# Performance work log

Measured on AMD Instinct MI355X. Metric: run time of the kernel, lower is better.

Reference implementation:

```python
import jax, jax.numpy as jnp
import numpy as np

B, T, D = 4, 2048, 1024
H, Kd = 4, 256                 # num_heads, head_k_dim
Vd = 512                       # head_v_dim = head_dim * expand_v
KEY_DIM, VAL_DIM = H * Kd, H * Vd
CONV = 4
EPS = 1e-6
LN_EPS = 1e-5


def _layernorm(x, g, b):
    m = jnp.mean(x, -1, keepdims=True)
    v = jnp.mean((x - m) ** 2, -1, keepdims=True)
    return (x - m) * jax.lax.rsqrt(v + LN_EPS) * g + b


def _rmsnorm(x, w):
    return x * jax.lax.rsqrt(jnp.mean(x * x, -1, keepdims=True) + EPS) * w


def _l2norm(x):
    return x * jax.lax.rsqrt(jnp.sum(x * x, -1, keepdims=True) + EPS)


def _causal_conv_silu(x, w):
    # depthwise causal conv: x [B,T,C], w [C,CONV]; y[t] = sum_i w[:,i]*x[t-(CONV-1)+i]
    t = x.shape[1]
    xp = jnp.pad(x, ((0, 0), (CONV - 1, 0), (0, 0)))
    y = xp[:, 0:t, :] * w[:, 0]
    for i in range(1, CONV):
        y = y + xp[:, i:i + t, :] * w[:, i]
    return jax.nn.silu(y)


def _gated_delta_rule(q, k, v, g, beta):
    # q,k [B,T,H,Kd] (l2-normed, q pre-scaled), v [B,T,H,Vd], g,beta [B,T,H]
    qT = jnp.moveaxis(q, 1, 0)
    kT = jnp.moveaxis(k, 1, 0)
    vT = jnp.moveaxis(v, 1, 0)
    gT = jnp.moveaxis(g, 1, 0)
    bT = jnp.moveaxis(beta, 1, 0)
    S0 = jnp.zeros((q.shape[0], H, Kd, Vd), q.dtype)

    def step(S, inp):
        q_t, k_t, v_t, g_t, b_t = inp
        S = S * jnp.exp(g_t)[..., None, None]          # decay state
        kv = jnp.einsum('bhk,bhkv->bhv', k_t, S)       # read old memory at k
        delta = (v_t - kv) * b_t[..., None]            # delta-rule update
        S = S + k_t[..., :, None] * delta[..., None, :]
        o = jnp.einsum('bhk,bhkv->bhv', q_t, S)
        return S, o

    _, o = jax.lax.scan(step, S0, (qT, kT, vT, gT, bT))
    return jnp.moveaxis(o, 0, 1)                       # [B,T,H,Vd]


def _forward(x, ln1_g, ln1_b, ln2_g, ln2_b, rms_in_w, Wq, Wk, Wv,
             conv_q_w, conv_k_w, conv_v_w, Wa, dt_bias, A_log, Wb,
             Wg, o_norm_w, Wo, W2, b2):
    b, t, _ = x.shape
    h = _layernorm(x, ln1_g, ln1_b)          # EncoderBlock norm_layer_1
    h = _rmsnorm(h, rms_in_w)                # GatedDeltaNet norm_first

    q = _causal_conv_silu(h @ Wq, conv_q_w).reshape(b, t, H, Kd)
    k = _causal_conv_silu(h @ Wk, conv_k_w).reshape(b, t, H, Kd)
    v = _causal_conv_silu(h @ Wv, conv_v_w).reshape(b, t, H, Vd)

    q = _l2norm(q) * (Kd ** -0.5)
    k = _l2norm(k)

    g = -jnp.exp(A_log) * jax.nn.softplus(h @ Wa + dt_bias)   # [B,T,H], log-decay
    beta = jax.nn.sigmoid(h @ Wb)                              # [B,T,H]

    o = _gated_delta_rule(q, k, v, g, beta)                    # [B,T,H,Vd]

    gate = (h @ Wg).reshape(b, t, H, Vd)
    o = _rmsnorm(o, o_norm_w) * jax.nn.silu(gate)              # gated RMSNorm output
    enc = o.reshape(b, t, VAL_DIM) @ Wo                        # o_proj

    x = x + enc                                                # residual
    h2 = _layernorm(x, ln2_g, ln2_b)
    x_out = jax.nn.gelu(h2 @ W2 + b2, approximate=False) + x   # stage 2 + residual
    return x_out


def setup_inputs() -> dict:
    key = jax.random.key(0)
    ks = jax.random.split(key, 16)
    r = lambda k, shp, s=0.02: jax.random.normal(k, shp, dtype=jnp.float32) * s
    return {
        'x': jax.random.normal(ks[0], (B, T, D), dtype=jnp.float32),
        'ln1_g': jnp.ones((D,), jnp.float32), 'ln1_b': jnp.zeros((D,), jnp.float32),
        'ln2_g': jnp.ones((D,), jnp.float32), 'ln2_b': jnp.zeros((D,), jnp.float32),
        'rms_in_w': jnp.ones((D,), jnp.float32),
        'Wq': r(ks[1], (D, KEY_DIM)), 'Wk': r(ks[2], (D, KEY_DIM)), 'Wv': r(ks[3], (D, VAL_DIM)),
        'conv_q_w': r(ks[4], (KEY_DIM, CONV), 0.3),
        'conv_k_w': r(ks[5], (KEY_DIM, CONV), 0.3),
        'conv_v_w': r(ks[6], (VAL_DIM, CONV), 0.3),
        'Wa': r(ks[7], (D, H)), 'dt_bias': r(ks[8], (H,), 0.5),
        'A_log': jnp.log(jax.random.uniform(ks[9], (H,), minval=1.0, maxval=16.0)),
        'Wb': r(ks[10], (D, H)),
        'Wg': r(ks[11], (D, VAL_DIM)),
        'o_norm_w': jnp.ones((Vd,), jnp.float32),
        'Wo': r(ks[12], (VAL_DIM, D)),
        'W2': r(ks[13], (D, D)), 'b2': jnp.zeros((D,), jnp.float32),
    }


def reference(x, ln1_g, ln1_b, ln2_g, ln2_b, rms_in_w, Wq, Wk, Wv,
              conv_q_w, conv_k_w, conv_v_w, Wa, dt_bias, A_log, Wb,
              Wg, o_norm_w, Wo, W2, b2):
    return _forward(x, ln1_g, ln1_b, ln2_g, ln2_b, rms_in_w, Wq, Wk, Wv,
                    conv_q_w, conv_k_w, conv_v_w, Wa, dt_bias, A_log, Wb,
                    Wg, o_norm_w, Wo, W2, b2)
```

## Files before the change

### kernel.cpp

```cpp
#include <hip/hip_runtime.h>
#include <stdint.h>

typedef uint16_t u16;
typedef __attribute__((ext_vector_type(8))) __bf16 bfrag8;
typedef __attribute__((ext_vector_type(4))) float f32x4;

#define DEV __device__ __forceinline__

DEV float bf2f(uint32_t lo16) { return __uint_as_float(lo16 << 16); }
DEV u16 f2bf(float f) {
  uint32_t u = __float_as_uint(f);
  u += 0x7fffu + ((u >> 16) & 1u);
  return (u16)(u >> 16);
}
DEV uint32_t pack2(float a, float b) { return (uint32_t)f2bf(a) | ((uint32_t)f2bf(b) << 16); }
DEV float sigmoidf_(float x) { return 1.f / (1.f + __expf(-x)); }

DEV float blk_sum(float v, float* sred, int tid) {
#pragma unroll
  for (int m = 32; m >= 1; m >>= 1) v += __shfl_xor(v, m);
  __syncthreads();
  if ((tid & 63) == 0) sred[tid >> 6] = v;
  __syncthreads();
  return sred[0] + sred[1] + sred[2] + sred[3];
}

__global__ __launch_bounds__(256) void transpose_w(const float* __restrict__ W,
                                                   u16* __restrict__ WT, int Kd_, int Nd_) {
  __shared__ float tile[32][33];
  int tx = threadIdx.x, ty = threadIdx.y;
  int n0 = blockIdx.x * 32, k0 = blockIdx.y * 32;
#pragma unroll
  for (int i = ty; i < 32; i += 8) tile[i][tx] = W[(size_t)(k0 + i) * Nd_ + n0 + tx];
  __syncthreads();
#pragma unroll
  for (int i = ty; i < 32; i += 8) WT[(size_t)(n0 + i) * Kd_ + k0 + tx] = f2bf(tile[tx][i]);
}

__global__ __launch_bounds__(256) void k1_kernel(
    const float* __restrict__ x, const float* __restrict__ ln1g, const float* __restrict__ ln1b,
    const float* __restrict__ rmsw, const float* __restrict__ Wa, const float* __restrict__ Wb,
    const float* __restrict__ dtb, const float* __restrict__ Alog,
    u16* __restrict__ hbf, float2* __restrict__ gb2) {
  __shared__ float sred[4];
  int row = blockIdx.x, tid = threadIdx.x;
  const float4 xv = ((const float4*)(x + (size_t)row * 1024))[tid];
  float ts  = blk_sum(xv.x + xv.y + xv.z + xv.w, sred, tid);
  float ts2 = blk_sum(xv.x * xv.x + xv.y * xv.y + xv.z * xv.z + xv.w * xv.w, sred, tid);
  float mean = ts * (1.f / 1024.f);
  float var  = ts2 * (1.f / 1024.f) - mean * mean;
  float inv  = rsqrtf(var + 1e-5f);
  int c = tid * 4;
  float l0 = (xv.x - mean) * inv * ln1g[c + 0] + ln1b[c + 0];
  float l1 = (xv.y - mean) * inv * ln1g[c + 1] + ln1b[c + 1];
  float l2 = (xv.z - mean) * inv * ln1g[c + 2] + ln1b[c + 2];
  float l3 = (xv.w - mean) * inv * ln1g[c + 3] + ln1b[c + 3];
  float ssq = blk_sum(l0 * l0 + l1 * l1 + l2 * l2 + l3 * l3, sred, tid);
  float rinv = rsqrtf(ssq * (1.f / 1024.f) + 1e-6f);
  float h0 = l0 * rinv * rmsw[c + 0];
  float h1 = l1 * rinv * rmsw[c + 1];
  float h2 = l2 * rinv * rmsw[c + 2];
  float h3 = l3 * rinv * rmsw[c + 3];
  uint2 pk;
  pk.x = pack2(h0, h1);
  pk.y = pack2(h2, h3);
  *(uint2*)(hbf + (size_t)row * 1024 + c) = pk;
  float hv[4] = {h0, h1, h2, h3};
  float pa[4] = {0, 0, 0, 0}, pb[4] = {0, 0, 0, 0};
#pragma unroll
  for (int e = 0; e < 4; e++) {
    const float* wa = Wa + (size_t)(c + e) * 4;
    const float* wb = Wb + (size_t)(c + e) * 4;
#pragma unroll
    for (int p = 0; p < 4; p++) {
      pa[p] = fmaf(hv[e], wa[p], pa[p]);
      pb[p] = fmaf(hv[e], wb[p], pb[p]);
    }
  }
  float ra[4], rb[4];
  for (int p = 0; p < 4; p++) ra[p] = blk_sum(pa[p], sred, tid);
  for (int p = 0; p < 4; p++) rb[p] = blk_sum(pb[p], sred, tid);
  if (tid < 4) {
    float z = ra[tid] + dtb[tid];
    float sp = fmaxf(z, 0.f) + log1pf(expf(-fabsf(z)));
    float2 o2;
    o2.x = -expf(Alog[tid]) * sp;
    o2.y = 1.f / (1.f + expf(-rb[tid]));
    gb2[(size_t)row * 4 + tid] = o2;
  }
}

template <int MODE>
__global__ __launch_bounds__(256) void gemm_bt(
    const u16* __restrict__ A, const u16* __restrict__ Bt, int M, int N, int K,
    float* __restrict__ outf, u16* __restrict__ outh,
    const float* __restrict__ res, const float* __restrict__ bias) {
  __shared__ u16 As[128 * 64];
  __shared__ u16 Bs[128 * 64];
  const int tid = threadIdx.x;
  const int lane = tid & 63;
  const int wv = tid >> 6;
  const int quad = lane >> 4;
  const int l16 = lane & 15;
  const int waveM = (wv & 1) * 64;
  const int waveN = (wv >> 1) * 64;
  const size_t arow0 = (size_t)blockIdx.y * 128;
  const size_t brow0 = (size_t)blockIdx.x * 128;
  const int srow = tid >> 3;
  const int soff = (tid & 7) * 8;
  f32x4 acc[4][4];
#pragma unroll
  for (int i = 0; i < 4; i++)
#pragma unroll
    for (int j = 0; j < 4; j++) acc[i][j] = (f32x4){0.f, 0.f, 0.f, 0.f};

  for (int k0 = 0; k0 < K; k0 += 64) {
    __syncthreads();
#pragma unroll
    for (int i = 0; i < 4; i++) {
      int r = i * 32 + srow;
      *(int4*)(As + r * 64 + soff) = *(const int4*)(A + (arow0 + r) * K + k0 + soff);
      *(int4*)(Bs + r * 64 + soff) = *(const int4*)(Bt + (brow0 + r) * K + k0 + soff);
    }
    __syncthreads();
#pragma unroll
    for (int kk = 0; kk < 2; kk++) {
      bfrag8 af[4], bfr[4];
#pragma unroll
      for (int i = 0; i < 4; i++) {
        af[i]  = *(const bfrag8*)(As + (waveM + i * 16 + l16) * 64 + kk * 32 + quad * 8);
        bfr[i] = *(const bfrag8*)(Bs + (waveN + i * 16 + l16) * 64 + kk * 32 + quad * 8);
      }
#pragma unroll
      for (int i = 0; i < 4; i++)
#pragma unroll
        for (int j = 0; j < 4; j++)
          acc[i][j] = __builtin_amdgcn_mfma_f32_16x16x32_bf16(af[i], bfr[j], acc[i][j], 0, 0, 0);
    }
  }
#pragma unroll
  for (int i = 0; i < 4; i++) {
    int r0 = (int)arow0 + waveM + i * 16 + quad * 4;
#pragma unroll
    for (int j = 0; j < 4; j++) {
      int cN = (int)brow0 + waveN + j * 16 + l16;
#pragma unroll
      for (int r = 0; r < 4; r++) {
        size_t idx = (size_t)(r0 + r) * N + cN;
        float vacc = acc[i][j][r];
        if (MODE == 0) {
          outh[idx] = f2bf(vacc);
        } else if (MODE == 1) {
          outf[idx] = vacc + res[idx];
        } else {
          float z = vacc + bias[cN];
          float ge = 0.5f * z * (1.f + erff(z * 0.70710678118654752f));
          outf[idx] = ge + res[idx];
        }
      }
    }
  }
}

__global__ __launch_bounds__(256) void conv_qk_kernel(
    const u16* __restrict__ qkv, const float* __restrict__ cwq, const float* __restrict__ cwk,
    u16* __restrict__ qf, u16* __restrict__ kf) {
  __shared__ float sred[4];
  int row = blockIdx.x, tid = threadIdx.x;
  int t = row & 2047;
  int isK = (blockIdx.y >= 4);
  int hh = blockIdx.y & 3;
  int c = hh * 256 + tid;
  const float* cw = isK ? cwk : cwq;
  int col = (isK ? 1024 : 0) + c;
  float acc = 0.f;
#pragma unroll
  for (int i = 0; i < 4; i++) {
    int tt = t - 3 + i;
    if (tt >= 0) acc = fmaf(cw[c * 4 + i], bf2f(qkv[(size_t)(row - 3 + i) * 4096 + col]), acc);
  }
  float y = acc * sigmoidf_(acc);
  float ssq = blk_sum(y * y, sred, tid);
  float r = rsqrtf(ssq + 1e-6f);
  float outv = y * r * (isK ? 1.f : 0.0625f);
  (isK ? kf : qf)[(size_t)row * 1024 + c] = f2bf(outv);
}

__global__ __launch_bounds__(256) void conv_v_kernel(
    const u16* __restrict__ qkv, const float* __restrict__ cwv, u16* __restrict__ vf) {
  int row = blockIdx.x, tid = threadIdx.x;
  int t = row & 2047;
  int c0 = blockIdx.y * 1024 + tid * 4;
  float a0 = 0, a1 = 0, a2 = 0, a3 = 0;
#pragma unroll
  for (int i = 0; i < 4; i++) {
    int tt = t - 3 + i;
    if (tt >= 0) {
      uint2 raw = *(const uint2*)(qkv + (size_t)(row - 3 + i) * 4096 + 2048 + c0);
      a0 = fmaf(cwv[(c0 + 0) * 4 + i], bf2f(raw.x & 0xffffu), a0);
      a1 = fmaf(cwv[(c0 + 1) * 4 + i], bf2f(raw.x >> 16), a1);
      a2 = fmaf(cwv[(c0 + 2) * 4 + i], bf2f(raw.y & 0xffffu), a2);
      a3 = fmaf(cwv[(c0 + 3) * 4 + i], bf2f(raw.y >> 16), a3);
    }
  }
  a0 = a0 * sigmoidf_(a0);
  a1 = a1 * sigmoidf_(a1);
  a2 = a2 * sigmoidf_(a2);
  a3 = a3 * sigmoidf_(a3);
  uint2 pk;
  pk.x = pack2(a0, a1);
  pk.y = pack2(a2, a3);
  *(uint2*)(vf + (size_t)row * 2048 + c0) = pk;
}


__global__ __launch_bounds__(256) void phaseA_kernel(
    const u16* __restrict__ kf, const u16* __restrict__ qf, const float2* __restrict__ gb2,
    u16* __restrict__ KTg, u16* __restrict__ Bg, u16* __restrict__ Mg,
    float2* __restrict__ gpk) {
  __shared__ uint8_t sm[51456];
  float* Nl  = (float*)sm;
  float* gl  = (float*)(sm + 16896);
  float* bl  = (float*)(sm + 17152);
  float* GL  = (float*)(sm + 17408);
  u16*  Klds = (u16*)(sm + 17664);
  float* Ml  = (float*)(sm + 17664);

  const int tid = threadIdx.x;
  const int lane = tid & 63;
  const int wv = tid >> 6;
  const int quad = lane >> 4;
  const int l16 = lane & 15;
  const int bh = blockIdx.x >> 5;
  const int ch = blockIdx.x & 31;
  const int b = bh >> 2, h = bh & 3;
  const int gr0 = b * 2048 + ch * 64;
  const size_t cid = (size_t)blockIdx.x;
  const size_t cid2 = (size_t)bh * 32 + ch;

  if (tid < 64) {
    float2 gv = gb2[(size_t)(gr0 + tid) * 4 + h];
    gl[tid] = gv.x; bl[tid] = gv.y;
  }
  __syncthreads();
  if (tid < 64) {
    float s = 0.f;
    for (int j = 0; j < 64; j++) { if (j <= tid) s += gl[j]; }
    GL[tid] = s;
  }
  {
    int r = tid >> 2, p = tid & 3;
    const u16* src = kf + (size_t)(gr0 + r) * 1024 + h * 256 + p * 64;
#pragma unroll
    for (int it = 0; it < 8; it++)
      *(uint4*)&Klds[r * 264 + p * 64 + it * 8] = *(const uint4*)(src + it * 8);
  }
  f32x4 ap[4], aq4[4];
#pragma unroll
  for (int nt = 0; nt < 4; nt++) { ap[nt] = (f32x4){0, 0, 0, 0}; aq4[nt] = (f32x4){0, 0, 0, 0}; }
  for (int ks = 0; ks < 8; ks++) {
    bfrag8 afk = *(const bfrag8*)(kf + (size_t)(gr0 + 16 * wv + l16) * 1024 + h * 256 + ks * 32 + quad * 8);
    bfrag8 afq = *(const bfrag8*)(qf + (size_t)(gr0 + 16 * wv + l16) * 1024 + h * 256 + ks * 32 + quad * 8);
#pragma unroll
    for (int nt = 0; nt < 4; nt++) {
      bfrag8 bfk = *(const bfrag8*)(kf + (size_t)(gr0 + 16 * nt + l16) * 1024 + h * 256 + ks * 32 + quad * 8);
      ap[nt]  = __builtin_amdgcn_mfma_f32_16x16x32_bf16(afk, bfk, ap[nt], 0, 0, 0);
      aq4[nt] = __builtin_amdgcn_mfma_f32_16x16x32_bf16(afq, bfk, aq4[nt], 0, 0, 0);
    }
  }
  __syncthreads();
#pragma unroll
  for (int nt = 0; nt < 4; nt++) {
#pragma unroll
    for (int r = 0; r < 4; r++) {
      int i = 16 * wv + quad * 4 + r;
      int j = 16 * nt + l16;
      float e = __expf(GL[i] - GL[j]);
      Nl[i * 66 + j] = (j < i) ? bl[i] * e * ap[nt][r] : 0.f;
      float bvv = (j <= i) ? e * aq4[nt][r] : 0.f;
      Bg[cid2 * 4096 + i * 64 + j] = f2bf(bvv);
    }
  }
  for (int e = 0; e < 64; e++) {
    int idx = e * 256 + tid;
    int i2 = idx & 63, k2 = idx >> 6;
    KTg[cid2 * 16384 + (size_t)k2 * 64 + i2] = Klds[i2 * 264 + k2];
  }
  if (tid < 64) {
    float2 gp;
    gp.x = __expf(GL[tid]);
    gp.y = __expf(GL[63] - GL[tid]);
    gpk[cid2 * 64 + tid] = gp;
  }
  __syncthreads();
  if (tid < 64) {
    int c = tid;
    for (int i = 0; i < 64; i++) {
      float acc = (i == c) ? bl[i] : 0.f;
      for (int j = 0; j < i; j++) acc -= Nl[i * 66 + j] * Ml[j * 66 + c];
      Ml[i * 66 + c] = acc;
    }
  }
  __syncthreads();
  for (int e = 0; e < 16; e++) {
    int idx = e * 256 + tid;
    int i2 = idx >> 6, j2 = idx & 63;
    Mg[cid2 * 4096 + i2 * 64 + j2] = f2bf(Ml[i2 * 66 + j2]);
  }
  (void)cid;
}

__global__ __launch_bounds__(256) void phaseB_kernel(
    const u16* __restrict__ kf, const u16* __restrict__ qf, const u16* __restrict__ vf,
    const u16* __restrict__ KTg, const u16* __restrict__ Bg, const u16* __restrict__ Mg,
    const float2* __restrict__ gpk, u16* __restrict__ obuf) {
  __shared__ u16 S0T[32 * 264];
  __shared__ u16 rhsT[32 * 72];
  __shared__ u16 dT[32 * 72];
  __shared__ u16 dhT[32 * 72];
  __shared__ float gin_s[64], gout_s[64];

  const int tid = threadIdx.x;
  const int lane = tid & 63;
  const int wv = tid >> 6;
  const int quad = lane >> 4;
  const int l16 = lane & 15;
  const int bh = blockIdx.x >> 4;
  const int sl = blockIdx.x & 15;
  const int b = bh >> 2, h = bh & 3;

  f32x4 S[8];
#pragma unroll
  for (int t = 0; t < 8; t++) S[t] = (f32x4){0, 0, 0, 0};

  for (int ch = 0; ch < 32; ch++) {
    const size_t cid = (size_t)bh * 32 + ch;
    const int gr0 = b * 2048 + ch * 64;
    const u16* kfc = kf + (size_t)gr0 * 1024 + h * 256;
    const u16* qfc = qf + (size_t)gr0 * 1024 + h * 256;
    const u16* vfc = vf + (size_t)gr0 * 2048 + h * 512 + sl * 32;
    u16* oc = obuf + (size_t)gr0 * 2048 + h * 512 + sl * 32;
    const u16* KTc = KTg + cid * 16384;
    const u16* Mc  = Mg + cid * 4096;
    const u16* Bc  = Bg + cid * 4096;

    if (tid < 64) {
      float2 gp = gpk[cid * 64 + tid];
      gin_s[tid] = gp.x; gout_s[tid] = gp.y;
    }
#pragma unroll
    for (int kt = 0; kt < 4; kt++)
#pragma unroll
      for (int nt = 0; nt < 2; nt++) {
        int k = wv * 64 + kt * 16 + quad * 4;
        int n = nt * 16 + l16;
        f32x4 sv = S[kt * 2 + nt];
        uint2 pk;
        pk.x = pack2(sv[0], sv[1]);
        pk.y = pack2(sv[2], sv[3]);
        *(uint2*)&S0T[n * 264 + k] = pk;
      }
    __syncthreads();

    f32x4 ar[2] = {(f32x4){0, 0, 0, 0}, (f32x4){0, 0, 0, 0}};
    for (int ks = 0; ks < 8; ks++) {
      bfrag8 af = *(const bfrag8*)(kfc + (size_t)(16 * wv + l16) * 1024 + ks * 32 + quad * 8);
#pragma unroll
      for (int nt = 0; nt < 2; nt++) {
        bfrag8 bf = *(const bfrag8*)&S0T[(nt * 16 + l16) * 264 + ks * 32 + quad * 8];
        ar[nt] = __builtin_amdgcn_mfma_f32_16x16x32_bf16(af, bf, ar[nt], 0, 0, 0);
      }
    }
#pragma unroll
    for (int nt = 0; nt < 2; nt++) {
      float rv[4];
#pragma unroll
      for (int r = 0; r < 4; r++) {
        int i = 16 * wv + quad * 4 + r;
        float vvv = bf2f(vfc[(size_t)i * 2048 + nt * 16 + l16]);
        rv[r] = vvv - gin_s[i] * ar[nt][r];
      }
      uint2 pk;
      pk.x = pack2(rv[0], rv[1]);
      pk.y = pack2(rv[2], rv[3]);
      *(uint2*)&rhsT[(nt * 16 + l16) * 72 + 16 * wv + quad * 4] = pk;
    }
    __syncthreads();

    f32x4 ad[2] = {(f32x4){0, 0, 0, 0}, (f32x4){0, 0, 0, 0}};
    for (int ks = 0; ks < 2; ks++) {
      bfrag8 af = *(const bfrag8*)(Mc + (size_t)(16 * wv + l16) * 64 + ks * 32 + quad * 8);
#pragma unroll
      for (int nt = 0; nt < 2; nt++) {
        bfrag8 bf = *(const bfrag8*)&rhsT[(nt * 16 + l16) * 72 + ks * 32 + quad * 8];
        ad[nt] = __builtin_amdgcn_mfma_f32_16x16x32_bf16(af, bf, ad[nt], 0, 0, 0);
      }
    }
#pragma unroll
    for (int nt = 0; nt < 2; nt++) {
      int i0 = 16 * wv + quad * 4;
      uint2 pk;
      pk.x = pack2(ad[nt][0], ad[nt][1]);
      pk.y = pack2(ad[nt][2], ad[nt][3]);
      *(uint2*)&dT[(nt * 16 + l16) * 72 + i0] = pk;
      uint2 pk2;
      pk2.x = pack2(gout_s[i0] * ad[nt][0], gout_s[i0 + 1] * ad[nt][1]);
      pk2.y = pack2(gout_s[i0 + 2] * ad[nt][2], gout_s[i0 + 3] * ad[nt][3]);
      *(uint2*)&dhT[(nt * 16 + l16) * 72 + i0] = pk2;
    }
    __syncthreads();

    f32x4 ao[2] = {(f32x4){0, 0, 0, 0}, (f32x4){0, 0, 0, 0}};
    for (int ks = 0; ks < 2; ks++) {
      bfrag8 af = *(const bfrag8*)(Bc + (size_t)(16 * wv + l16) * 64 + ks * 32 + quad * 8);
#pragma unroll
      for (int nt = 0; nt < 2; nt++) {
        bfrag8 bf = *(const bfrag8*)&dT[(nt * 16 + l16) * 72 + ks * 32 + quad * 8];
        ao[nt] = __builtin_amdgcn_mfma_f32_16x16x32_bf16(af, bf, ao[nt], 0, 0, 0);
      }
    }
    f32x4 aq[2] = {(f32x4){0, 0, 0, 0}, (f32x4){0, 0, 0, 0}};
    for (int ks = 0; ks < 8; ks++) {
      bfrag8 af = *(const bfrag8*)(qfc + (size_t)(16 * wv + l16) * 1024 + ks * 32 + quad * 8);
#pragma unroll
      for (int nt = 0; nt < 2; nt++) {
        bfrag8 bf = *(const bfrag8*)&S0T[(nt * 16 + l16) * 264 + ks * 32 + quad * 8];
        aq[nt] = __builtin_amdgcn_mfma_f32_16x16x32_bf16(af, bf, aq[nt], 0, 0, 0);
      }
    }
#pragma unroll
    for (int nt = 0; nt < 2; nt++)
#pragma unroll
      for (int r = 0; r < 4; r++) {
        int i = 16 * wv + quad * 4 + r;
        float ov = gin_s[i] * aq[nt][r] + ao[nt][r];
        oc[(size_t)i * 2048 + nt * 16 + l16] = f2bf(ov);
      }

    float gC = gin_s[63];
#pragma unroll
    for (int kt = 0; kt < 4; kt++) {
      f32x4 c0 = S[kt * 2] * gC;
      f32x4 c1 = S[kt * 2 + 1] * gC;
      for (int ks = 0; ks < 2; ks++) {
        bfrag8 af = *(const bfrag8*)(KTc + (size_t)(wv * 64 + kt * 16 + l16) * 64 + ks * 32 + quad * 8);
        bfrag8 bf0 = *(const bfrag8*)&dhT[(0 * 16 + l16) * 72 + ks * 32 + quad * 8];
        bfrag8 bf1 = *(const bfrag8*)&dhT[(1 * 16 + l16) * 72 + ks * 32 + quad * 8];
        c0 = __builtin_amdgcn_mfma_f32_16x16x32_bf16(af, bf0, c0, 0, 0, 0);
        c1 = __builtin_amdgcn_mfma_f32_16x16x32_bf16(af, bf1, c1, 0, 0, 0);
      }
      S[kt * 2] = c0;
      S[kt * 2 + 1] = c1;
    }
    __syncthreads();
  }
}

__global__ __launch_bounds__(256) void onorm_kernel(
    const u16* __restrict__ o, const u16* __restrict__ gate,
    const float* __restrict__ onw, u16* __restrict__ ofin) {
  __shared__ float sred[4];
  int row = blockIdx.x, hh = blockIdx.y, tid = threadIdx.x;
  size_t base = (size_t)row * 2048 + hh * 512;
  uint32_t oraw = *(const uint32_t*)(o + base + tid * 2);
  float o0 = bf2f(oraw & 0xffffu), o1 = bf2f(oraw >> 16);
  float ssq = blk_sum(o0 * o0 + o1 * o1, sred, tid);
  float rinv = rsqrtf(ssq * (1.f / 512.f) + 1e-6f);
  uint32_t graw = *(const uint32_t*)(gate + base + tid * 2);
  float g0 = bf2f(graw & 0xffffu), g1 = bf2f(graw >> 16);
  float r0 = o0 * rinv * onw[tid * 2 + 0] * (g0 * sigmoidf_(g0));
  float r1 = o1 * rinv * onw[tid * 2 + 1] * (g1 * sigmoidf_(g1));
  *(uint32_t*)(ofin + base + tid * 2) = pack2(r0, r1);
}

__global__ __launch_bounds__(256) void ln2_kernel(
    const float* __restrict__ x1, const float* __restrict__ g2, const float* __restrict__ b2,
    u16* __restrict__ h2) {
  __shared__ float sred[4];
  int row = blockIdx.x, tid = threadIdx.x;
  const float4 xv = ((const float4*)(x1 + (size_t)row * 1024))[tid];
  float ts  = blk_sum(xv.x + xv.y + xv.z + xv.w, sred, tid);
  float ts2 = blk_sum(xv.x * xv.x + xv.y * xv.y + xv.z * xv.z + xv.w * xv.w, sred, tid);
  float mean = ts * (1.f / 1024.f);
  float inv = rsqrtf(ts2 * (1.f / 1024.f) - mean * mean + 1e-5f);
  int c = tid * 4;
  float h0 = (xv.x - mean) * inv * g2[c + 0] + b2[c + 0];
  float h1 = (xv.y - mean) * inv * g2[c + 1] + b2[c + 1];
  float h2v = (xv.z - mean) * inv * g2[c + 2] + b2[c + 2];
  float h3 = (xv.w - mean) * inv * g2[c + 3] + b2[c + 3];
  uint2 pk;
  pk.x = pack2(h0, h1);
  pk.y = pack2(h2v, h3);
  *(uint2*)(h2 + (size_t)row * 1024 + c) = pk;
}

extern "C" void kernel_launch(void* const* d_in, const int* in_sizes, int n_in,
                              void* d_out, int out_size, void* d_ws, size_t ws_size,
                              hipStream_t stream) {
  (void)in_sizes; (void)n_in; (void)out_size; (void)ws_size;
  const float* x    = (const float*)d_in[0];
  const float* ln1g = (const float*)d_in[1];
  const float* ln1b = (const float*)d_in[2];
  const float* ln2g = (const float*)d_in[3];
  const float* ln2b = (const float*)d_in[4];
  const float* rmsw = (const float*)d_in[5];
  const float* Wq   = (const float*)d_in[6];
  const float* Wk   = (const float*)d_in[7];
  const float* Wv   = (const float*)d_in[8];
  const float* cwq  = (const float*)d_in[9];
  const float* cwk  = (const float*)d_in[10];
  const float* cwv  = (const float*)d_in[11];
  const float* Wa   = (const float*)d_in[12];
  const float* dtb  = (const float*)d_in[13];
  const float* Alog = (const float*)d_in[14];
  const float* Wb   = (const float*)d_in[15];
  const float* Wg   = (const float*)d_in[16];
  const float* onw  = (const float*)d_in[17];
  const float* Wo   = (const float*)d_in[18];
  const float* W2   = (const float*)d_in[19];
  const float* b2   = (const float*)d_in[20];

  uint8_t* ws = (uint8_t*)d_ws;
  const size_t MB = 1024ull * 1024;
  u16*   qkvp  = (u16*)(ws);
  u16*   obuf  = (u16*)(ws);
  u16*   KTg   = (u16*)(ws + 32 * MB);
  u16*   Bg    = (u16*)(ws + 48 * MB);
  u16*   Mg    = (u16*)(ws + 52 * MB);
  float2* gpk  = (float2*)(ws + 56 * MB);
  u16*   gate  = (u16*)(ws + 32 * MB);
  u16*   hbf   = (u16*)(ws + 64 * MB);
  u16*   WTqkv = (u16*)(ws + 80 * MB);
  u16*   WgT   = (u16*)(ws + 88 * MB);
  u16*   WoT   = (u16*)(ws + 92 * MB);
  u16*   W2T   = (u16*)(ws + 96 * MB);
  u16*   qf    = (u16*)(ws + 98 * MB);
  u16*   kf    = (u16*)(ws + 114 * MB);
  u16*   vf    = (u16*)(ws + 130 * MB);
  u16*   ofin  = (u16*)(ws + 98 * MB);
  u16*   h2bf  = (u16*)(ws + 130 * MB);
  float2* gb2  = (float2*)(ws + 162 * MB);
  float* x1    = (float*)d_out;
  float* outp  = (float*)d_out;

  dim3 tb(32, 8);
  transpose_w<<<dim3(32, 32), tb, 0, stream>>>(Wq, WTqkv,               1024, 1024);
  transpose_w<<<dim3(32, 32), tb, 0, stream>>>(Wk, WTqkv + 1024 * 1024, 1024, 1024);
  transpose_w<<<dim3(64, 32), tb, 0, stream>>>(Wv, WTqkv + 2048 * 1024, 1024, 2048);
  transpose_w<<<dim3(64, 32), tb, 0, stream>>>(Wg, WgT,                 1024, 2048);
  transpose_w<<<dim3(32, 64), tb, 0, stream>>>(Wo, WoT,                 2048, 1024);
  transpose_w<<<dim3(32, 32), tb, 0, stream>>>(W2, W2T,                 1024, 1024);

  k1_kernel<<<8192, 256, 0, stream>>>(x, ln1g, ln1b, rmsw, Wa, Wb, dtb, Alog, hbf, gb2);
  gemm_bt<0><<<dim3(32, 64), 256, 0, stream>>>(hbf, WTqkv, 8192, 4096, 1024, nullptr, qkvp, nullptr, nullptr);
  conv_qk_kernel<<<dim3(8192, 8), 256, 0, stream>>>(qkvp, cwq, cwk, qf, kf);
  conv_v_kernel<<<dim3(8192, 2), 256, 0, stream>>>(qkvp, cwv, vf);
  phaseA_kernel<<<512, 256, 0, stream>>>(kf, qf, gb2, KTg, Bg, Mg, gpk);
  phaseB_kernel<<<256, 256, 0, stream>>>(kf, qf, vf, KTg, Bg, Mg, gpk, obuf);
  gemm_bt<0><<<dim3(16, 64), 256, 0, stream>>>(hbf, WgT, 8192, 2048, 1024, nullptr, gate, nullptr, nullptr);
  onorm_kernel<<<dim3(8192, 4), 256, 0, stream>>>(obuf, gate, onw, ofin);
  gemm_bt<1><<<dim3(8, 64), 256, 0, stream>>>(ofin, WoT, 8192, 1024, 2048, x1, nullptr, x, nullptr);
  ln2_kernel<<<8192, 256, 0, stream>>>(x1, ln2g, ln2b, h2bf);
  gemm_bt<2><<<dim3(8, 64), 256, 0, stream>>>(h2bf, W2T, 8192, 1024, 1024, outp, nullptr, x1, b2);
}
```

Before: 922.9 us.

## Split phaseB value columns across more blocks and use direct global-to-LDS loads in GEMM

The chunked delta-rule recurrence kernel now gives each block 16 value columns instead of 32, doubling the grid from 256 to 512 blocks. This halves per-block registers and LDS so more of the GPU's compute units are busy during the serial scan over chunks. The cost is that every block re-reads the same k/q/KT/M/B chunk data twice as often. Separately, the tiled GEMM replaces register-staged int4 copies with global_load_lds intrinsics that write straight into LDS, cutting VGPR use and copy instructions.

```diff
diff --git a/kernel.cpp b/kernel.cpp
--- a/kernel.cpp
+++ b/kernel.cpp
@@ -15,6 +15,12 @@
 }
 DEV uint32_t pack2(float a, float b) { return (uint32_t)f2bf(a) | ((uint32_t)f2bf(b) << 16); }
 DEV float sigmoidf_(float x) { return 1.f / (1.f + __expf(-x)); }
+
+DEV void g2lds16(const u16* g, u16* l) {
+  __builtin_amdgcn_global_load_lds(
+      (const __attribute__((address_space(1))) void*)g,
+      (__attribute__((address_space(3))) void*)l, 16, 0, 0);
+}
 
 DEV float blk_sum(float v, float* sred, int tid) {
 #pragma unroll
@@ -119,8 +125,8 @@
 #pragma unroll
     for (int i = 0; i < 4; i++) {
       int r = i * 32 + srow;
-      *(int4*)(As + r * 64 + soff) = *(const int4*)(A + (arow0 + r) * K + k0 + soff);
-      *(int4*)(Bs + r * 64 + soff) = *(const int4*)(Bt + (brow0 + r) * K + k0 + soff);
+      g2lds16(A + (arow0 + r) * K + k0 + soff, As + r * 64 + soff);
+      g2lds16(Bt + (brow0 + r) * K + k0 + soff, Bs + r * 64 + soff);
     }
     __syncthreads();
 #pragma unroll
@@ -235,7 +241,6 @@
   const int ch = blockIdx.x & 31;
   const int b = bh >> 2, h = bh & 3;
   const int gr0 = b * 2048 + ch * 64;
-  const size_t cid = (size_t)blockIdx.x;
   const size_t cid2 = (size_t)bh * 32 + ch;
 
   if (tid < 64) {
@@ -307,17 +312,16 @@
     int i2 = idx >> 6, j2 = idx & 63;
     Mg[cid2 * 4096 + i2 * 64 + j2] = f2bf(Ml[i2 * 66 + j2]);
   }
-  (void)cid;
 }
 
 __global__ __launch_bounds__(256) void phaseB_kernel(
     const u16* __restrict__ kf, const u16* __restrict__ qf, const u16* __restrict__ vf,
     const u16* __restrict__ KTg, const u16* __restrict__ Bg, const u16* __restrict__ Mg,
     const float2* __restrict__ gpk, u16* __restrict__ obuf) {
-  __shared__ u16 S0T[32 * 264];
-  __shared__ u16 rhsT[32 * 72];
-  __shared__ u16 dT[32 * 72];
-  __shared__ u16 dhT[32 * 72];
+  __shared__ u16 S0T[16 * 264];
+  __shared__ u16 rhsT[16 * 72];
+  __shared__ u16 dT[16 * 72];
+  __shared__ u16 dhT[16 * 72];
   __shared__ float gin_s[64], gout_s[64];
 
   const int tid = threadIdx.x;
@@ -325,21 +329,21 @@
   const int wv = tid >> 6;
   const int quad = lane >> 4;
   const int l16 = lane & 15;
-  const int bh = blockIdx.x >> 4;
-  const int sl = blockIdx.x & 15;
+  const int bh = blockIdx.x >> 5;
+  const int sl = blockIdx.x & 31;
   const int b = bh >> 2, h = bh & 3;
 
-  f32x4 S[8];
-#pragma unroll
-  for (int t = 0; t < 8; t++) S[t] = (f32x4){0, 0, 0, 0};
+  f32x4 S[4];
+#pragma unroll
+  for (int t = 0; t < 4; t++) S[t] = (f32x4){0, 0, 0, 0};
 
   for (int ch = 0; ch < 32; ch++) {
     const size_t cid = (size_t)bh * 32 + ch;
     const int gr0 = b * 2048 + ch * 64;
     const u16* kfc = kf + (size_t)gr0 * 1024 + h * 256;
     const u16* qfc = qf + (size_t)gr0 * 1024 + h * 256;
-    const u16* vfc = vf + (size_t)gr0 * 2048 + h * 512 + sl * 32;
-    u16* oc = obuf + (size_t)gr0 * 2048 + h * 512 + sl * 32;
+    const u16* vfc = vf + (size_t)gr0 * 2048 + h * 512 + sl * 16;
+    u16* oc = obuf + (size_t)gr0 * 2048 + h * 512 + sl * 16;
     const u16* KTc = KTg + cid * 16384;
     const u16* Mc  = Mg + cid * 4096;
     const u16* Bc  = Bg + cid * 4096;
@@ -349,108 +353,85 @@
       gin_s[tid] = gp.x; gout_s[tid] = gp.y;
     }
 #pragma unroll
-    for (int kt = 0; kt < 4; kt++)
-#pragma unroll
-      for (int nt = 0; nt < 2; nt++) {
-        int k = wv * 64 + kt * 16 + quad * 4;
-        int n = nt * 16 + l16;
-        f32x4 sv = S[kt * 2 + nt];
-        uint2 pk;
-        pk.x = pack2(sv[0], sv[1]);
-        pk.y = pack2(sv[2], sv[3]);
-        *(uint2*)&S0T[n * 264 + k] = pk;
-      }
+    for (int kt = 0; kt < 4; kt++) {
+      int k = wv * 64 + kt * 16 + quad * 4;
+      f32x4 sv = S[kt];
+      uint2 pk;
+      pk.x = pack2(sv[0], sv[1]);
+      pk.y = pack2(sv[2], sv[3]);
+      *(uint2*)&S0T[l16 * 264 + k] = pk;
+    }
     __syncthreads();
 
-    f32x4 ar[2] = {(f32x4){0, 0, 0, 0}, (f32x4){0, 0, 0, 0}};
+    f32x4 ar = (f32x4){0, 0, 0, 0};
     for (int ks = 0; ks < 8; ks++) {
       bfrag8 af = *(const bfrag8*)(kfc + (size_t)(16 * wv + l16) * 1024 + ks * 32 + quad * 8);
-#pragma unroll
-      for (int nt = 0; nt < 2; nt++) {
-        bfrag8 bf = *(const bfrag8*)&S0T[(nt * 16 + l16) * 264 + ks * 32 + quad * 8];
-        ar[nt] = __builtin_amdgcn_mfma_f32_16x16x32_bf16(af, bf, ar[nt], 0, 0, 0);
-      }
-    }
-#pragma unroll
-    for (int nt = 0; nt < 2; nt++) {
+      bfrag8 bf = *(const bfrag8*)&S0T[l16 * 264 + ks * 32 + quad * 8];
+      ar = __builtin_amdgcn_mfma_f32_16x16x32_bf16(af, bf, ar, 0, 0, 0);
+    }
+    {
       float rv[4];
 #pragma unroll
       for (int r = 0; r < 4; r++) {
         int i = 16 * wv + quad * 4 + r;
-        float vvv = bf2f(vfc[(size_t)i * 2048 + nt * 16 + l16]);
-        rv[r] = vvv - gin_s[i] * ar[nt][r];
+        float vvv = bf2f(vfc[(size_t)i * 2048 + l16]);
+        rv[r] = vvv - gin_s[i] * ar[r];
       }
       uint2 pk;
       pk.x = pack2(rv[0], rv[1]);
       pk.y = pack2(rv[2], rv[3]);
-      *(uint2*)&rhsT[(nt * 16 + l16) * 72 + 16 * wv + quad * 4] = pk;
+      *(uint2*)&rhsT[l16 * 72 + 16 * wv + quad * 4] = pk;
     }
     __syncthreads();
 
-    f32x4 ad[2] = {(f32x4){0, 0, 0, 0}, (f32x4){0, 0, 0, 0}};
+    f32x4 ad = (f32x4){0, 0, 0, 0};
     for (int ks = 0; ks < 2; ks++) {
       bfrag8 af = *(const bfrag8*)(Mc + (size_t)(16 * wv + l16) * 64 + ks * 32 + quad * 8);
-#pragma unroll
-      for (int nt = 0; nt < 2; nt++) {
-        bfrag8 bf = *(const bfrag8*)&rhsT[(nt * 16 + l16) * 72 + ks * 32 + quad * 8];
-        ad[nt] = __builtin_amdgcn_mfma_f32_16x16x32_bf16(af, bf, ad[nt], 0, 0, 0);
-      }
-    }
-#pragma unroll
-    for (int nt = 0; nt < 2; nt++) {
+      bfrag8 bf = *(const bfrag8*)&rhsT[l16 * 72 + ks * 32 + quad * 8];
+      ad = __builtin_amdgcn_mfma_f32_16x16x32_bf16(af, bf, ad, 0, 0, 0);
+    }
+    {
       int i0 = 16 * wv + quad * 4;
       uint2 pk;
-      pk.x = pack2(ad[nt][0], ad[nt][1]);
-      pk.y = pack2(ad[nt][2], ad[nt][3]);
-      *(uint2*)&dT[(nt * 16 + l16) * 72 + i0] = pk;
+      pk.x = pack2(ad[0], ad[1]);
+      pk.y = pack2(ad[2], ad[3]);
+      *(uint2*)&dT[l16 * 72 + i0] = pk;
       uint2 pk2;
-      pk2.x = pack2(gout_s[i0] * ad[nt][0], gout_s[i0 + 1] * ad[nt][1]);
-      pk2.y = pack2(gout_s[i0 + 2] * ad[nt][2], gout_s[i0 + 3] * ad[nt][3]);
-      *(uint2*)&dhT[(nt * 16 + l16) * 72 + i0] = pk2;
+      pk2.x = pack2(gout_s[i0] * ad[0], gout_s[i0 + 1] * ad[1]);
+      pk2.y = pack2(gout_s[i0 + 2] * ad[2], gout_s[i0 + 3] * ad[3]);
+      *(uint2*)&dhT[l16 * 72 + i0] = pk2;
     }
     __syncthreads();
 
-    f32x4 ao[2] = {(f32x4){0, 0, 0, 0}, (f32x4){0, 0, 0, 0}};
+    f32x4 ao = (f32x4){0, 0, 0, 0};
     for (int ks = 0; ks < 2; ks++) {
       bfrag8 af = *(const bfrag8*)(Bc + (size_t)(16 * wv + l16) * 64 + ks * 32 + quad * 8);
-#pragma unroll
-      for (int nt = 0; nt < 2; nt++) {
-        bfrag8 bf = *(const bfrag8*)&dT[(nt * 16 + l16) * 72 + ks * 32 + quad * 8];
-        ao[nt] = __builtin_amdgcn_mfma_f32_16x16x32_bf16(af, bf, ao[nt], 0, 0, 0);
-      }
-    }
-    f32x4 aq[2] = {(f32x4){0, 0, 0, 0}, (f32x4){0, 0, 0, 0}};
+      bfrag8 bf = *(const bfrag8*)&dT[l16 * 72 + ks * 32 + quad * 8];
+      ao = __builtin_amdgcn_mfma_f32_16x16x32_bf16(af, bf, ao, 0, 0, 0);
+    }
+    f32x4 aq = (f32x4){0, 0, 0, 0};
     for (int ks = 0; ks < 8; ks++) {
       bfrag8 af = *(const bfrag8*)(qfc + (size_t)(16 * wv + l16) * 1024 + ks * 32 + quad * 8);
-#pragma unroll
-      for (int nt = 0; nt < 2; nt++) {
-        bfrag8 bf = *(const bfrag8*)&S0T[(nt * 16 + l16) * 264 + ks * 32 + quad * 8];
-        aq[nt] = __builtin_amdgcn_mfma_f32_16x16x32_bf16(af, bf, aq[nt], 0, 0, 0);
-      }
-    }
-#pragma unroll
-    for (int nt = 0; nt < 2; nt++)
-#pragma unroll
-      for (int r = 0; r < 4; r++) {
-        int i = 16 * wv + quad * 4 + r;
-        float ov = gin_s[i] * aq[nt][r] + ao[nt][r];
-        oc[(size_t)i * 2048 + nt * 16 + l16] = f2bf(ov);
-      }
+      bfrag8 bf = *(const bfrag8*)&S0T[l16 * 264 + ks * 32 + quad * 8];
+      aq = __builtin_amdgcn_mfma_f32_16x16x32_bf16(af, bf, aq, 0, 0, 0);
+    }
+#pragma unroll
+    for (int r = 0; r < 4; r++) {
+      int i = 16 * wv + quad * 4 + r;
+      float ov = gin_s[i] * aq[r] + ao[r];
+      oc[(size_t)i * 2048 + l16] = f2bf(ov);
+    }
 
     float gC = gin_s[63];
 #pragma unroll
     for (int kt = 0; kt < 4; kt++) {
-      f32x4 c0 = S[kt * 2] * gC;
-      f32x4 c1 = S[kt * 2 + 1] * gC;
+      f32x4 c0 = S[kt] * gC;
       for (int ks = 0; ks < 2; ks++) {
         bfrag8 af = *(const bfrag8*)(KTc + (size_t)(wv * 64 + kt * 16 + l16) * 64 + ks * 32 + quad * 8);
-        bfrag8 bf0 = *(const bfrag8*)&dhT[(0 * 16 + l16) * 72 + ks * 32 + quad * 8];
-        bfrag8 bf1 = *(const bfrag8*)&dhT[(1 * 16 + l16) * 72 + ks * 32 + quad * 8];
-        c0 = __builtin_amdgcn_mfma_f32_16x16x32_bf16(af, bf0, c0, 0, 0, 0);
-        c1 = __builtin_amdgcn_mfma_f32_16x16x32_bf16(af, bf1, c1, 0, 0, 0);
+        bfrag8 bf = *(const bfrag8*)&dhT[l16 * 72 + ks * 32 + quad * 8];
+        c0 = __builtin_amdgcn_mfma_f32_16x16x32_bf16(af, bf, c0, 0, 0, 0);
       }
-      S[kt * 2] = c0;
-      S[kt * 2 + 1] = c1;
+      S[kt] = c0;
     }
     __syncthreads();
   }
@@ -556,7 +537,7 @@
   conv_qk_kernel<<<dim3(8192, 8), 256, 0, stream>>>(qkvp, cwq, cwk, qf, kf);
   conv_v_kernel<<<dim3(8192, 2), 256, 0, stream>>>(qkvp, cwv, vf);
   phaseA_kernel<<<512, 256, 0, stream>>>(kf, qf, gb2, KTg, Bg, Mg, gpk);
-  phaseB_kernel<<<256, 256, 0, stream>>>(kf, qf, vf, KTg, Bg, Mg, gpk, obuf);
+  phaseB_kernel<<<512, 256, 0, stream>>>(kf, qf, vf, KTg, Bg, Mg, gpk, obuf);
   gemm_bt<0><<<dim3(16, 64), 256, 0, stream>>>(hbf, WgT, 8192, 2048, 1024, nullptr, gate, nullptr, nullptr);
   onorm_kernel<<<dim3(8192, 4), 256, 0, stream>>>(obuf, gate, onw, ofin);
   gemm_bt<1><<<dim3(8, 64), 256, 0, stream>>>(ofin, WoT, 8192, 1024, 2048, x1, nullptr, x, nullptr);
```

Measured after the change: 926.3 us. Within noise of the previous version (+0.4%).

## Prefetch next chunk operands into registers and fold decay into K^T in delta-rule scan

Applied to the files above, without the earlier changes.

The chunked delta-rule scan kernel now loads every per-chunk operand (k, q, K^T, M, B fragments, v values, gates) for chunk c+1 into registers while chunk c is being computed. This hides global-memory latency on the serial chunk loop. The gout decay is folded into K^T during preprocessing, which removes the dhT LDS buffer and one write pass. The q·S and k·S products are fused into one loop, and the trailing barrier is dropped. The GEMM tile loads switch to direct global-to-LDS loads. The prefetch roughly doubles register pressure, which may reduce occupancy or cause spills, and removing the end-of-loop sync relies on the next barrier for correctness.

```diff
diff --git a/kernel.cpp b/kernel.cpp
--- a/kernel.cpp
+++ b/kernel.cpp
@@ -15,6 +15,12 @@
 }
 DEV uint32_t pack2(float a, float b) { return (uint32_t)f2bf(a) | ((uint32_t)f2bf(b) << 16); }
 DEV float sigmoidf_(float x) { return 1.f / (1.f + __expf(-x)); }
+
+DEV void g2lds16(const u16* g, u16* l) {
+  __builtin_amdgcn_global_load_lds(
+      (const __attribute__((address_space(1))) void*)g,
+      (__attribute__((address_space(3))) void*)l, 16, 0, 0);
+}
 
 DEV float blk_sum(float v, float* sred, int tid) {
 #pragma unroll
@@ -119,8 +125,8 @@
 #pragma unroll
     for (int i = 0; i < 4; i++) {
       int r = i * 32 + srow;
-      *(int4*)(As + r * 64 + soff) = *(const int4*)(A + (arow0 + r) * K + k0 + soff);
-      *(int4*)(Bs + r * 64 + soff) = *(const int4*)(Bt + (brow0 + r) * K + k0 + soff);
+      g2lds16(A + (arow0 + r) * K + k0 + soff, As + r * 64 + soff);
+      g2lds16(Bt + (brow0 + r) * K + k0 + soff, Bs + r * 64 + soff);
     }
     __syncthreads();
 #pragma unroll
@@ -235,7 +241,6 @@
   const int ch = blockIdx.x & 31;
   const int b = bh >> 2, h = bh & 3;
   const int gr0 = b * 2048 + ch * 64;
-  const size_t cid = (size_t)blockIdx.x;
   const size_t cid2 = (size_t)bh * 32 + ch;
 
   if (tid < 64) {
@@ -281,10 +286,14 @@
       Bg[cid2 * 4096 + i * 64 + j] = f2bf(bvv);
     }
   }
-  for (int e = 0; e < 64; e++) {
-    int idx = e * 256 + tid;
-    int i2 = idx & 63, k2 = idx >> 6;
-    KTg[cid2 * 16384 + (size_t)k2 * 64 + i2] = Klds[i2 * 264 + k2];
+  {
+    float GC = GL[63];
+    for (int e = 0; e < 64; e++) {
+      int idx = e * 256 + tid;
+      int i2 = idx & 63, k2 = idx >> 6;
+      float kv = bf2f(Klds[i2 * 264 + k2]) * __expf(GC - GL[i2]);
+      KTg[cid2 * 16384 + (size_t)k2 * 64 + i2] = f2bf(kv);
+    }
   }
   if (tid < 64) {
     float2 gp;
@@ -307,7 +316,40 @@
     int i2 = idx >> 6, j2 = idx & 63;
     Mg[cid2 * 4096 + i2 * 64 + j2] = f2bf(Ml[i2 * 66 + j2]);
   }
-  (void)cid;
+}
+
+struct OpsB {
+  bfrag8 kf8[8], qf8[8], kt8[8], m2[2], b2f[2];
+  u16 vv[8];
+  float gin[4], gC;
+};
+
+DEV void loadOpsB(OpsB& o, const u16* kfc, const u16* qfc, const u16* vfc,
+                  const u16* KTc, const u16* Mc, const u16* Bc,
+                  const float2* gpc, int wv, int l16, int quad, int i0) {
+#pragma unroll
+  for (int ks = 0; ks < 8; ks++) {
+    o.kf8[ks] = *(const bfrag8*)(kfc + (size_t)(16 * wv + l16) * 1024 + ks * 32 + quad * 8);
+    o.qf8[ks] = *(const bfrag8*)(qfc + (size_t)(16 * wv + l16) * 1024 + ks * 32 + quad * 8);
+  }
+#pragma unroll
+  for (int kt = 0; kt < 4; kt++)
+#pragma unroll
+    for (int ks = 0; ks < 2; ks++)
+      o.kt8[kt * 2 + ks] = *(const bfrag8*)(KTc + (size_t)(64 * wv + kt * 16 + l16) * 64 + ks * 32 + quad * 8);
+#pragma unroll
+  for (int ks = 0; ks < 2; ks++) {
+    o.m2[ks]  = *(const bfrag8*)(Mc + (size_t)(16 * wv + l16) * 64 + ks * 32 + quad * 8);
+    o.b2f[ks] = *(const bfrag8*)(Bc + (size_t)(16 * wv + l16) * 64 + ks * 32 + quad * 8);
+  }
+#pragma unroll
+  for (int nt = 0; nt < 2; nt++)
+#pragma unroll
+    for (int r = 0; r < 4; r++)
+      o.vv[nt * 4 + r] = vfc[(size_t)(i0 + r) * 2048 + nt * 16 + l16];
+#pragma unroll
+  for (int r = 0; r < 4; r++) o.gin[r] = gpc[i0 + r].x;
+  o.gC = gpc[63].x;
 }
 
 __global__ __launch_bounds__(256) void phaseB_kernel(
@@ -317,8 +359,6 @@
   __shared__ u16 S0T[32 * 264];
   __shared__ u16 rhsT[32 * 72];
   __shared__ u16 dT[32 * 72];
-  __shared__ u16 dhT[32 * 72];
-  __shared__ float gin_s[64], gout_s[64];
 
   const int tid = threadIdx.x;
   const int lane = tid & 63;
@@ -328,131 +368,118 @@
   const int bh = blockIdx.x >> 4;
   const int sl = blockIdx.x & 15;
   const int b = bh >> 2, h = bh & 3;
+  const int i0 = quad * 4;
 
   f32x4 S[8];
 #pragma unroll
   for (int t = 0; t < 8; t++) S[t] = (f32x4){0, 0, 0, 0};
 
+  const size_t cidb = (size_t)bh * 32;
+  const u16* kfb = kf + ((size_t)b * 2048) * 1024 + h * 256;
+  const u16* qfb = qf + ((size_t)b * 2048) * 1024 + h * 256;
+  const u16* vfb = vf + ((size_t)b * 2048) * 2048 + h * 512 + sl * 32;
+  u16* ob = obuf + ((size_t)b * 2048) * 2048 + h * 512 + sl * 32;
+
+  OpsB cur, nxt;
+  loadOpsB(cur, kfb, qfb, vfb, KTg + cidb * 16384, Mg + cidb * 4096, Bg + cidb * 4096,
+           gpk + cidb * 64, wv, l16, quad, 16 * wv + i0);
+
   for (int ch = 0; ch < 32; ch++) {
-    const size_t cid = (size_t)bh * 32 + ch;
-    const int gr0 = b * 2048 + ch * 64;
-    const u16* kfc = kf + (size_t)gr0 * 1024 + h * 256;
-    const u16* qfc = qf + (size_t)gr0 * 1024 + h * 256;
-    const u16* vfc = vf + (size_t)gr0 * 2048 + h * 512 + sl * 32;
-    u16* oc = obuf + (size_t)gr0 * 2048 + h * 512 + sl * 32;
-    const u16* KTc = KTg + cid * 16384;
-    const u16* Mc  = Mg + cid * 4096;
-    const u16* Bc  = Bg + cid * 4096;
-
-    if (tid < 64) {
-      float2 gp = gpk[cid * 64 + tid];
-      gin_s[tid] = gp.x; gout_s[tid] = gp.y;
-    }
+    if (ch < 31) {
+      int c1 = ch + 1;
+      loadOpsB(nxt, kfb + (size_t)c1 * 64 * 1024, qfb + (size_t)c1 * 64 * 1024,
+               vfb + (size_t)c1 * 64 * 2048, KTg + (cidb + c1) * 16384,
+               Mg + (cidb + c1) * 4096, Bg + (cidb + c1) * 4096,
+               gpk + (cidb + c1) * 64, wv, l16, quad, 16 * wv + i0);
+    }
+    u16* oc = ob + (size_t)ch * 64 * 2048;
+
 #pragma unroll
     for (int kt = 0; kt < 4; kt++)
 #pragma unroll
       for (int nt = 0; nt < 2; nt++) {
-        int k = wv * 64 + kt * 16 + quad * 4;
-        int n = nt * 16 + l16;
+        int k = wv * 64 + kt * 16 + i0;
         f32x4 sv = S[kt * 2 + nt];
         uint2 pk;
         pk.x = pack2(sv[0], sv[1]);
         pk.y = pack2(sv[2], sv[3]);
-        *(uint2*)&S0T[n * 264 + k] = pk;
+        *(uint2*)&S0T[(nt * 16 + l16) * 264 + k] = pk;
       }
     __syncthreads();
 
     f32x4 ar[2] = {(f32x4){0, 0, 0, 0}, (f32x4){0, 0, 0, 0}};
+    f32x4 aq[2] = {(f32x4){0, 0, 0, 0}, (f32x4){0, 0, 0, 0}};
+#pragma unroll
     for (int ks = 0; ks < 8; ks++) {
-      bfrag8 af = *(const bfrag8*)(kfc + (size_t)(16 * wv + l16) * 1024 + ks * 32 + quad * 8);
-#pragma unroll
-      for (int nt = 0; nt < 2; nt++) {
-        bfrag8 bf = *(const bfrag8*)&S0T[(nt * 16 + l16) * 264 + ks * 32 + quad * 8];
-        ar[nt] = __builtin_amdgcn_mfma_f32_16x16x32_bf16(af, bf, ar[nt], 0, 0, 0);
-      }
+      bfrag8 b0 = *(const bfrag8*)&S0T[(0 * 16 + l16) * 264 + ks * 32 + quad * 8];
+      bfrag8 b1 = *(const bfrag8*)&S0T[(1 * 16 + l16) * 264 + ks * 32 + quad * 8];
+      ar[0] = __builtin_amdgcn_mfma_f32_16x16x32_bf16(cur.kf8[ks], b0, ar[0], 0, 0, 0);
+      ar[1] = __builtin_amdgcn_mfma_f32_16x16x32_bf16(cur.kf8[ks], b1, ar[1], 0, 0, 0);
+      aq[0] = __builtin_amdgcn_mfma_f32_16x16x32_bf16(cur.qf8[ks], b0, aq[0], 0, 0, 0);
+      aq[1] = __builtin_amdgcn_mfma_f32_16x16x32_bf16(cur.qf8[ks], b1, aq[1], 0, 0, 0);
     }
 #pragma unroll
     for (int nt = 0; nt < 2; nt++) {
       float rv[4];
 #pragma unroll
-      for (int r = 0; r < 4; r++) {
-        int i = 16 * wv + quad * 4 + r;
-        float vvv = bf2f(vfc[(size_t)i * 2048 + nt * 16 + l16]);
-        rv[r] = vvv - gin_s[i] * ar[nt][r];
-      }
+      for (int r = 0; r < 4; r++)
+        rv[r] = bf2f(cur.vv[nt * 4 + r]) - cur.gin[r] * ar[nt][r];
       uint2 pk;
       pk.x = pack2(rv[0], rv[1]);
       pk.y = pack2(rv[2], rv[3]);
-      *(uint2*)&rhsT[(nt * 16 + l16) * 72 + 16 * wv + quad * 4] = pk;
+      *(uint2*)&rhsT[(nt * 16 + l16) * 72 + 16 * wv + i0] = pk;
     }
     __syncthreads();
 
     f32x4 ad[2] = {(f32x4){0, 0, 0, 0}, (f32x4){0, 0, 0, 0}};
+#pragma unroll
     for (int ks = 0; ks < 2; ks++) {
-      bfrag8 af = *(const bfrag8*)(Mc + (size_t)(16 * wv + l16) * 64 + ks * 32 + quad * 8);
 #pragma unroll
       for (int nt = 0; nt < 2; nt++) {
         bfrag8 bf = *(const bfrag8*)&rhsT[(nt * 16 + l16) * 72 + ks * 32 + quad * 8];
-        ad[nt] = __builtin_amdgcn_mfma_f32_16x16x32_bf16(af, bf, ad[nt], 0, 0, 0);
+        ad[nt] = __builtin_amdgcn_mfma_f32_16x16x32_bf16(cur.m2[ks], bf, ad[nt], 0, 0, 0);
       }
     }
 #pragma unroll
     for (int nt = 0; nt < 2; nt++) {
-      int i0 = 16 * wv + quad * 4;
       uint2 pk;
       pk.x = pack2(ad[nt][0], ad[nt][1]);
       pk.y = pack2(ad[nt][2], ad[nt][3]);
-      *(uint2*)&dT[(nt * 16 + l16) * 72 + i0] = pk;
-      uint2 pk2;
-      pk2.x = pack2(gout_s[i0] * ad[nt][0], gout_s[i0 + 1] * ad[nt][1]);
-      pk2.y = pack2(gout_s[i0 + 2] * ad[nt][2], gout_s[i0 + 3] * ad[nt][3]);
-      *(uint2*)&dhT[(nt * 16 + l16) * 72 + i0] = pk2;
+      *(uint2*)&dT[(nt * 16 + l16) * 72 + 16 * wv + i0] = pk;
     }
     __syncthreads();
 
     f32x4 ao[2] = {(f32x4){0, 0, 0, 0}, (f32x4){0, 0, 0, 0}};
+#pragma unroll
     for (int ks = 0; ks < 2; ks++) {
-      bfrag8 af = *(const bfrag8*)(Bc + (size_t)(16 * wv + l16) * 64 + ks * 32 + quad * 8);
 #pragma unroll
       for (int nt = 0; nt < 2; nt++) {
         bfrag8 bf = *(const bfrag8*)&dT[(nt * 16 + l16) * 72 + ks * 32 + quad * 8];
-        ao[nt] = __builtin_amdgcn_mfma_f32_16x16x32_bf16(af, bf, ao[nt], 0, 0, 0);
-      }
-    }
-    f32x4 aq[2] = {(f32x4){0, 0, 0, 0}, (f32x4){0, 0, 0, 0}};
-    for (int ks = 0; ks < 8; ks++) {
-      bfrag8 af = *(const bfrag8*)(qfc + (size_t)(16 * wv + l16) * 1024 + ks * 32 + quad * 8);
+        ao[nt] = __builtin_amdgcn_mfma_f32_16x16x32_bf16(cur.b2f[ks], bf, ao[nt], 0, 0, 0);
+      }
+    }
+#pragma unroll
+    for (int nt = 0; nt < 2; nt++)
+#pragma unroll
+      for (int r = 0; r < 4; r++) {
+        int i = 16 * wv + i0 + r;
+        float ov = cur.gin[r] * aq[nt][r] + ao[nt][r];
+        oc[(size_t)i * 2048 + nt * 16 + l16] = f2bf(ov);
+      }
+
+#pragma unroll
+    for (int kt = 0; kt < 4; kt++)
 #pragma unroll
       for (int nt = 0; nt < 2; nt++) {
-        bfrag8 bf = *(const bfrag8*)&S0T[(nt * 16 + l16) * 264 + ks * 32 + quad * 8];
-        aq[nt] = __builtin_amdgcn_mfma_f32_16x16x32_bf16(af, bf, aq[nt], 0, 0, 0);
-      }
-    }
-#pragma unroll
-    for (int nt = 0; nt < 2; nt++)
-#pragma unroll
-      for (int r = 0; r < 4; r++) {
-        int i = 16 * wv + quad * 4 + r;
-        float ov = gin_s[i] * aq[nt][r] + ao[nt][r];
-        oc[(size_t)i * 2048 + nt * 16 + l16] = f2bf(ov);
-      }
-
-    float gC = gin_s[63];
-#pragma unroll
-    for (int kt = 0; kt < 4; kt++) {
-      f32x4 c0 = S[kt * 2] * gC;
-      f32x4 c1 = S[kt * 2 + 1] * gC;
-      for (int ks = 0; ks < 2; ks++) {
-        bfrag8 af = *(const bfrag8*)(KTc + (size_t)(wv * 64 + kt * 16 + l16) * 64 + ks * 32 + quad * 8);
-        bfrag8 bf0 = *(const bfrag8*)&dhT[(0 * 16 + l16) * 72 + ks * 32 + quad * 8];
-        bfrag8 bf1 = *(const bfrag8*)&dhT[(1 * 16 + l16) * 72 + ks * 32 + quad * 8];
-        c0 = __builtin_amdgcn_mfma_f32_16x16x32_bf16(af, bf0, c0, 0, 0, 0);
-        c1 = __builtin_amdgcn_mfma_f32_16x16x32_bf16(af, bf1, c1, 0, 0, 0);
-      }
-      S[kt * 2] = c0;
-      S[kt * 2 + 1] = c1;
-    }
-    __syncthreads();
+        f32x4 c0 = S[kt * 2 + nt] * cur.gC;
+#pragma unroll
+        for (int ks = 0; ks < 2; ks++) {
+          bfrag8 bf = *(const bfrag8*)&dT[(nt * 16 + l16) * 72 + ks * 32 + quad * 8];
+          c0 = __builtin_amdgcn_mfma_f32_16x16x32_bf16(cur.kt8[kt * 2 + ks], bf, c0, 0, 0, 0);
+        }
+        S[kt * 2 + nt] = c0;
+      }
+    cur = nxt;
   }
 }
 
```

Measured after the change: 847.4 us. 1.09x faster.
